# Performance work log

Measured on AMD Instinct MI355X. Metric: run time of the kernel, lower is better.

The kernel has to match this reference:

```python
import jax, jax.numpy as jnp
import numpy as np

IMG_W, IMG_H = 960.0, 512.0  # image_size from cfg


def setup_inputs() -> dict:
    B, N, J = 4, 5, 15
    Hh, Wh = 128, 240
    rng = np.random.default_rng(0)
    heatmaps = jnp.asarray(rng.random((N, B, J, Hh, Wh)).astype(np.float32))
    # rotations near identity (orthonormalized, det=+1)
    A = np.eye(3, dtype=np.float32) + 0.05 * rng.normal(size=(B, N, 3, 3)).astype(np.float32)
    Q = np.linalg.qr(A)[0]
    det = np.linalg.det(Q)
    Q[..., :, 0] = Q[..., :, 0] * det[..., None]
    R = jnp.asarray(Q.astype(np.float32))
    # cameras ~5m behind the volume so cam-z > 0 everywhere
    T = jnp.asarray((np.array([0.0, 0.0, -5000.0], np.float32) + 100.0 * rng.normal(size=(B, N, 3))).astype(np.float32))
    f = jnp.asarray((1000.0 + 20.0 * rng.normal(size=(B, N, 2))).astype(np.float32))
    c = jnp.asarray(np.tile(np.array([IMG_W / 2, IMG_H / 2], np.float32), (B, N, 1)))
    trans = jnp.asarray(np.tile(np.array([[1.0, 0.0, 0.0], [0.0, 1.0, 0.0]], np.float32), (B, N, 1, 1)))
    wh = jnp.asarray(np.tile(np.array([IMG_W, IMG_H], np.float32), (B, N, 1)))  # width,height = center*2
    gc = np.stack([rng.uniform(-500, 500, B), rng.uniform(-500, 500, B), np.full(B, 1000.0)], axis=1).astype(np.float32)
    grid_center = jnp.asarray(gc)
    return dict(heatmaps=heatmaps, R=R, T=T, f=f, c=c, trans=trans, wh=wh,
                grid_center=grid_center, gs_x=8000, gs_y=8000, gs_z=2000,
                cb_x=80, cb_y=80, cb_z=20)


def _bilinear(img, g):
    # img [J,H,W], g [P,2] in normalized coords; align_corners=True, zero padding
    Jn, H, W = img.shape
    x = (g[:, 0] + 1.0) * 0.5 * (W - 1)
    y = (g[:, 1] + 1.0) * 0.5 * (H - 1)
    x0 = jnp.floor(x)
    y0 = jnp.floor(y)
    wx = x - x0
    wy = y - y0

    def gather(xi, yi):
        valid = ((xi >= 0) & (xi <= W - 1) & (yi >= 0) & (yi <= H - 1)).astype(img.dtype)
        xc = jnp.clip(xi, 0, W - 1).astype(jnp.int32)
        yc = jnp.clip(yi, 0, H - 1).astype(jnp.int32)
        return img[:, yc, xc] * valid  # [J,P]

    return (gather(x0, y0) * (1 - wx) * (1 - wy) + gather(x0 + 1, y0) * wx * (1 - wy)
            + gather(x0, y0 + 1) * (1 - wx) * wy + gather(x0 + 1, y0 + 1) * wx * wy)


def _forward(heatmaps, R, T, f, c, trans, wh, grid_center, gs_x, gs_y, gs_z, cb_x, cb_y, cb_z):
    N, B, J, Hh, Wh = heatmaps.shape
    P = cb_x * cb_y * cb_z
    # compute_grid: world-space voxel centers per batch
    gx = jnp.linspace(-gs_x / 2, gs_x / 2, cb_x)
    gy = jnp.linspace(-gs_y / 2, gs_y / 2, cb_y)
    gz = jnp.linspace(-gs_z / 2, gs_z / 2, cb_z)
    mx, my, mz = jnp.meshgrid(gx, gy, gz, indexing='ij')
    base = jnp.stack([mx.ravel(), my.ravel(), mz.ravel()], axis=-1).astype(jnp.float32)  # [P,3]
    grids = base[None] + grid_center[:, None, :]                                         # [B,P,3]
    # world_to_pixel (pinhole): cam = R (X - T); pixel = f*cam_xy/cam_z + c
    diff = grids[:, None, :, :] - T[:, :, None, :]              # [B,N,P,3]
    cam = jnp.einsum('bnij,bnpj->bnpi', R, diff)                # [B,N,P,3]
    xy = cam[..., :2] / cam[..., 2:3] * f[:, :, None, :] + c[:, :, None, :]  # [B,N,P,2]
    width = wh[..., 0][:, :, None]
    height = wh[..., 1][:, :, None]
    bound = ((xy[..., 0] >= 0) & (xy[..., 1] >= 0) &
             (xy[..., 0] < width) & (xy[..., 1] < height)).astype(jnp.float32)  # [B,N,P]
    maxwh = jnp.maximum(width, height)[..., None]
    xy = jnp.clip(xy, -1.0, maxwh)
    # affine transform to model-input frame, then rescale to heatmap frame
    xy = jnp.einsum('bnij,bnpj->bnpi', trans[..., :2], xy) + trans[..., 2][:, :, None, :]
    xy = xy * jnp.array([Wh, Hh], jnp.float32) / jnp.array([IMG_W, IMG_H], jnp.float32)
    sg = jnp.clip(xy / jnp.array([Wh - 1, Hh - 1], jnp.float32) * 2.0 - 1.0, -1.1, 1.1)  # [B,N,P,2]
    imgs = jnp.transpose(heatmaps, (1, 0, 2, 3, 4)).reshape(B * N, J, Hh, Wh)
    samples = jax.vmap(_bilinear)(imgs, sg.reshape(B * N, P, 2))   # [B*N,J,P]
    cubes = jnp.transpose(samples.reshape(B, N, J, P), (0, 2, 3, 1))  # [B,J,P,N]
    wmask = jnp.transpose(bound, (0, 2, 1))[:, None]                  # [B,1,P,N]
    fused = jnp.sum(cubes * wmask, axis=-1) / (jnp.sum(wmask, axis=-1) + 1e-6)  # [B,J,P]
    fused = jnp.where(jnp.isnan(fused), 0.0, fused)
    fused = jnp.clip(fused, 0.0, 1.0).reshape(B, J, cb_x, cb_y, cb_z)
    return fused, grids


def reference(heatmaps, R, T, f, c, trans, wh, grid_center, gs_x, gs_y, gs_z, cb_x, cb_y, cb_z):
    return _forward(heatmaps, R, T, f, c, trans, wh, grid_center,
                    gs_x, gs_y, gs_z, cb_x, cb_y, cb_z)
```

## Files before the change

### kernel.cpp

```cpp
#include <hip/hip_runtime.h>
#include <hip/hip_fp16.h>

#define BB   4
#define NN   5
#define JJ   15
#define HHH  128
#define WHH  240
#define CBX  80
#define CBY  80
#define CBZ  20
#define PP   (CBX*CBY*CBZ)
#define HW   (HHH*WHH)
#define IMGW 960.0f
#define IMGH 512.0f
#define RECU 16


__global__ __launch_bounds__(256) void pack_kernel(
    const float* __restrict__ hm, unsigned int* __restrict__ ws)
{
    __shared__ float rows[JJ][WHH + 1];
    int bid = blockIdx.x;
    int n = bid % NN;
    int y = (bid / NN) % HHH;
    int b = bid / (NN * HHH);

    const float* src = hm + ((size_t)(n * BB + b) * JJ) * HW + y * WHH;
    for (int idx = threadIdx.x; idx < JJ * (WHH + 1); idx += 256) {
        int j = idx / (WHH + 1);
        int x = idx - j * (WHH + 1);
        int xs = min(x, WHH - 1);
        rows[j][x] = src[j * HW + xs];
    }
    __syncthreads();

    unsigned int* dst = ws + (size_t)((b * HHH + y) * NN + n) * WHH * RECU;
    for (int idx = threadIdx.x; idx < WHH * RECU; idx += 256) {
        int x = idx >> 4;
        int u = idx & 15;
        unsigned int val = 0u;
        if (u < JJ) {
            __half2 h = __halves2half2(__float2half_rn(rows[u][x]),
                                       __float2half_rn(rows[u][x + 1]));
            val = *reinterpret_cast<unsigned int*>(&h);
        }
        dst[idx] = val;
    }
}

__global__ __launch_bounds__(256) void project_kernel(
    const unsigned int* __restrict__ ws,
    const float* __restrict__ Rm,
    const float* __restrict__ Tv,
    const float* __restrict__ fv,
    const float* __restrict__ cv,
    const float* __restrict__ trans,
    const float* __restrict__ whv,
    const float* __restrict__ gcv,
    float* __restrict__ out)
{
    int t = blockIdx.x * blockDim.x + threadIdx.x;
    if (t >= BB * PP) return;
    int b = t / PP;
    int p = t - b * PP;
    int ix  = p / (CBY * CBZ);
    int rem = p - ix * (CBY * CBZ);
    int iy  = rem / CBZ;
    int iz  = rem - iy * CBZ;

    const float stx = 8000.0f / (CBX - 1);
    const float sty = 8000.0f / (CBY - 1);
    const float stz = 2000.0f / (CBZ - 1);
    float gx = -4000.0f + (float)ix * stx + gcv[b * 3 + 0];
    float gy = -4000.0f + (float)iy * sty + gcv[b * 3 + 1];
    float gz = -1000.0f + (float)iz * stz + gcv[b * 3 + 2];

    {
        float* grids_out = out + (size_t)BB * JJ * PP;
        size_t gb = (size_t)(b * PP + p) * 3;
        grids_out[gb + 0] = gx;
        grids_out[gb + 1] = gy;
        grids_out[gb + 2] = gz;
    }

    float cl0[NN], cr0[NN], cl1[NN], cr1[NN];
    int   r0[NN], r1[NN];
    float bnd[NN];
    float sumb = 0.0f;

    #pragma unroll
    for (int n = 0; n < NN; ++n) {
        int bn = b * NN + n;
        const float* R = Rm + bn * 9;
        float dx = gx - Tv[bn * 3 + 0];
        float dy = gy - Tv[bn * 3 + 1];
        float dz = gz - Tv[bn * 3 + 2];
        float cx = R[0] * dx + R[1] * dy + R[2] * dz;
        float cy = R[3] * dx + R[4] * dy + R[5] * dz;
        float cz = R[6] * dx + R[7] * dy + R[8] * dz;
        float inv = 1.0f / cz;
        float px = cx * inv * fv[bn * 2 + 0] + cv[bn * 2 + 0];
        float py = cy * inv * fv[bn * 2 + 1] + cv[bn * 2 + 1];
        float w = whv[bn * 2 + 0], h = whv[bn * 2 + 1];
        float bound = (px >= 0.0f && py >= 0.0f && px < w && py < h) ? 1.0f : 0.0f;
        float mwh = fmaxf(w, h);
        px = fminf(fmaxf(px, -1.0f), mwh);
        py = fminf(fmaxf(py, -1.0f), mwh);
        const float* tr = trans + bn * 6;
        float tx = tr[0] * px + tr[1] * py + tr[2];
        float ty = tr[3] * px + tr[4] * py + tr[5];
        tx *= (float)WHH / IMGW;
        ty *= (float)HHH / IMGH;
        float sgx = tx / (float)(WHH - 1) * 2.0f - 1.0f;
        float sgy = ty / (float)(HHH - 1) * 2.0f - 1.0f;
        sgx = fminf(fmaxf(sgx, -1.1f), 1.1f);
        sgy = fminf(fmaxf(sgy, -1.1f), 1.1f);
        float xx = (sgx + 1.0f) * 0.5f * (float)(WHH - 1);
        float yy = (sgy + 1.0f) * 0.5f * (float)(HHH - 1);
        float x0f = floorf(xx), y0f = floorf(yy);
        float wx = xx - x0f, wy = yy - y0f;
        int x0 = (int)x0f, y0 = (int)y0f;

        float axl, axr; int xb;
        if (x0 < 0) {
            axl = (x0 == -1) ? wx : 0.0f; axr = 0.0f; xb = 0;
        } else if (x0 >= WHH - 1) {
            axl = (x0 == WHH - 1) ? (1.0f - wx) : 0.0f; axr = 0.0f; xb = WHH - 1;
        } else {
            axl = 1.0f - wx; axr = wx; xb = x0;
        }

        float vy0 = (y0 >= 0 && y0 <= HHH - 1) ? 1.0f : 0.0f;
        float vy1 = (y0 + 1 >= 0 && y0 + 1 <= HHH - 1) ? 1.0f : 0.0f;
        int yc0 = min(max(y0, 0), HHH - 1);
        int yc1 = min(max(y0 + 1, 0), HHH - 1);
        float ay0 = (1.0f - wy) * vy0 * bound;
        float ay1 = wy * vy1 * bound;

        cl0[n] = axl * ay0;  cr0[n] = axr * ay0;
        cl1[n] = axl * ay1;  cr1[n] = axr * ay1;
        r0[n] = ((((b * HHH + yc0) * NN + n) * WHH) + xb) * RECU;
        r1[n] = ((((b * HHH + yc1) * NN + n) * WHH) + xb) * RECU;
        bnd[n] = bound;
        sumb += bound;
    }

    float acc[JJ];
    #pragma unroll
    for (int j = 0; j < JJ; ++j) acc[j] = 0.0f;

    #pragma unroll
    for (int n = 0; n < NN; ++n) {
        if (bnd[n] != 0.0f) {
            const uint4* q0 = reinterpret_cast<const uint4*>(ws + r0[n]);
            const uint4* q1 = reinterpret_cast<const uint4*>(ws + r1[n]);
            uint4 a0 = q0[0], a1 = q0[1], a2 = q0[2], a3 = q0[3];
            uint4 b0 = q1[0], b1 = q1[1], b2 = q1[2], b3 = q1[3];
            float c0l = cl0[n], c0r = cr0[n], c1l = cl1[n], c1r = cr1[n];
            unsigned int s0[16] = {a0.x,a0.y,a0.z,a0.w, a1.x,a1.y,a1.z,a1.w,
                                   a2.x,a2.y,a2.z,a2.w, a3.x,a3.y,a3.z,a3.w};
            unsigned int s1[16] = {b0.x,b0.y,b0.z,b0.w, b1.x,b1.y,b1.z,b1.w,
                                   b2.x,b2.y,b2.z,b2.w, b3.x,b3.y,b3.z,b3.w};
            #pragma unroll
            for (int j = 0; j < JJ; ++j) {
                __half2 h0 = *reinterpret_cast<__half2*>(&s0[j]);
                __half2 h1 = *reinterpret_cast<__half2*>(&s1[j]);
                float2 f0 = __half22float2(h0);
                float2 f1 = __half22float2(h1);
                acc[j] += c0l * f0.x + c0r * f0.y + c1l * f1.x + c1r * f1.y;
            }
        }
    }

    float denom = 1.0f / (sumb + 1e-6f);
    size_t outb = (size_t)b * JJ * PP + p;
    #pragma unroll
    for (int j = 0; j < JJ; ++j) {
        float v = acc[j] * denom;
        v = fminf(fmaxf(v, 0.0f), 1.0f);
        out[outb + (size_t)j * PP] = v;
    }
}

extern "C" void kernel_launch(void* const* d_in, const int* in_sizes, int n_in,
                              void* d_out, int out_size, void* d_ws, size_t ws_size,
                              hipStream_t stream) {
    const float* hm    = (const float*)d_in[0];
    const float* Rm    = (const float*)d_in[1];
    const float* Tv    = (const float*)d_in[2];
    const float* fv    = (const float*)d_in[3];
    const float* cv    = (const float*)d_in[4];
    const float* trans = (const float*)d_in[5];
    const float* whv   = (const float*)d_in[6];
    const float* gcv   = (const float*)d_in[7];
    float* out = (float*)d_out;
    unsigned int* ws = (unsigned int*)d_ws;

    pack_kernel<<<BB * HHH * NN, 256, 0, stream>>>(hm, ws);

    int total = BB * PP;
    int block = 256;
    int grid  = (total + block - 1) / block;
    project_kernel<<<grid, block, 0, stream>>>(ws, Rm, Tv, fv, cv, trans, whv, gcv, out);
}
```

Measured before the change: 153.5 us.

## Split joint channels across four threads per voxel in projection kernel

Each voxel is now handled by four threads, each responsible for four of the fifteen joint channels. Each thread loads one 16-byte vector per camera row instead of four. This cuts per-thread register pressure and raises the number of threads available to hide gather latency. In exchange, the projection math is repeated four times per voxel, and output stores become strided across lanes, since adjacent threads write different joint planes for the same voxel.

Measured after the change: 169.8 us. 10.7% more time.

```diff
diff --git a/kernel.cpp b/kernel.cpp
--- a/kernel.cpp
+++ b/kernel.cpp
@@ -59,10 +59,12 @@
     const float* __restrict__ gcv,
     float* __restrict__ out)
 {
-    int t = blockIdx.x * blockDim.x + threadIdx.x;
-    if (t >= BB * PP) return;
-    int b = t / PP;
-    int p = t - b * PP;
+    int tid = threadIdx.x;
+    int jg  = tid & 3;
+    int v   = tid >> 2;
+    int tvox = blockIdx.x * 64 + v;
+    int b = tvox / PP;
+    int p = tvox - b * PP;
     int ix  = p / (CBY * CBZ);
     int rem = p - ix * (CBY * CBZ);
     int iy  = rem / CBZ;
@@ -75,7 +77,7 @@
     float gy = -4000.0f + (float)iy * sty + gcv[b * 3 + 1];
     float gz = -1000.0f + (float)iz * stz + gcv[b * 3 + 2];
 
-    {
+    if (jg == 0) {
         float* grids_out = out + (size_t)BB * JJ * PP;
         size_t gb = (size_t)(b * PP + p) * 3;
         grids_out[gb + 0] = gx;
@@ -139,46 +141,53 @@
 
         cl0[n] = axl * ay0;  cr0[n] = axr * ay0;
         cl1[n] = axl * ay1;  cr1[n] = axr * ay1;
-        r0[n] = ((((b * HHH + yc0) * NN + n) * WHH) + xb) * RECU;
-        r1[n] = ((((b * HHH + yc1) * NN + n) * WHH) + xb) * RECU;
+        r0[n] = ((((b * HHH + yc0) * NN + n) * WHH) + xb) * RECU + jg * 4;
+        r1[n] = ((((b * HHH + yc1) * NN + n) * WHH) + xb) * RECU + jg * 4;
         bnd[n] = bound;
         sumb += bound;
     }
 
-    float acc[JJ];
-    #pragma unroll
-    for (int j = 0; j < JJ; ++j) acc[j] = 0.0f;
+    float acc0 = 0.0f, acc1 = 0.0f, acc2 = 0.0f, acc3 = 0.0f;
 
     #pragma unroll
     for (int n = 0; n < NN; ++n) {
         if (bnd[n] != 0.0f) {
-            const uint4* q0 = reinterpret_cast<const uint4*>(ws + r0[n]);
-            const uint4* q1 = reinterpret_cast<const uint4*>(ws + r1[n]);
-            uint4 a0 = q0[0], a1 = q0[1], a2 = q0[2], a3 = q0[3];
-            uint4 b0 = q1[0], b1 = q1[1], b2 = q1[2], b3 = q1[3];
+            uint4 a = *reinterpret_cast<const uint4*>(ws + r0[n]);
+            uint4 c = *reinterpret_cast<const uint4*>(ws + r1[n]);
             float c0l = cl0[n], c0r = cr0[n], c1l = cl1[n], c1r = cr1[n];
-            unsigned int s0[16] = {a0.x,a0.y,a0.z,a0.w, a1.x,a1.y,a1.z,a1.w,
-                                   a2.x,a2.y,a2.z,a2.w, a3.x,a3.y,a3.z,a3.w};
-            unsigned int s1[16] = {b0.x,b0.y,b0.z,b0.w, b1.x,b1.y,b1.z,b1.w,
-                                   b2.x,b2.y,b2.z,b2.w, b3.x,b3.y,b3.z,b3.w};
-            #pragma unroll
-            for (int j = 0; j < JJ; ++j) {
-                __half2 h0 = *reinterpret_cast<__half2*>(&s0[j]);
-                __half2 h1 = *reinterpret_cast<__half2*>(&s1[j]);
-                float2 f0 = __half22float2(h0);
-                float2 f1 = __half22float2(h1);
-                acc[j] += c0l * f0.x + c0r * f0.y + c1l * f1.x + c1r * f1.y;
-            }
+            float2 f;
+            f = __half22float2(*reinterpret_cast<__half2*>(&a.x));
+            acc0 += c0l * f.x + c0r * f.y;
+            f = __half22float2(*reinterpret_cast<__half2*>(&a.y));
+            acc1 += c0l * f.x + c0r * f.y;
+            f = __half22float2(*reinterpret_cast<__half2*>(&a.z));
+            acc2 += c0l * f.x + c0r * f.y;
+            f = __half22float2(*reinterpret_cast<__half2*>(&a.w));
+            acc3 += c0l * f.x + c0r * f.y;
+            f = __half22float2(*reinterpret_cast<__half2*>(&c.x));
+            acc0 += c1l * f.x + c1r * f.y;
+            f = __half22float2(*reinterpret_cast<__half2*>(&c.y));
+            acc1 += c1l * f.x + c1r * f.y;
+            f = __half22float2(*reinterpret_cast<__half2*>(&c.z));
+            acc2 += c1l * f.x + c1r * f.y;
+            f = __half22float2(*reinterpret_cast<__half2*>(&c.w));
+            acc3 += c1l * f.x + c1r * f.y;
         }
     }
 
     float denom = 1.0f / (sumb + 1e-6f);
     size_t outb = (size_t)b * JJ * PP + p;
-    #pragma unroll
-    for (int j = 0; j < JJ; ++j) {
-        float v = acc[j] * denom;
-        v = fminf(fmaxf(v, 0.0f), 1.0f);
-        out[outb + (size_t)j * PP] = v;
+    int j0 = jg * 4;
+    float vv;
+    vv = fminf(fmaxf(acc0 * denom, 0.0f), 1.0f);
+    out[outb + (size_t)(j0 + 0) * PP] = vv;
+    vv = fminf(fmaxf(acc1 * denom, 0.0f), 1.0f);
+    out[outb + (size_t)(j0 + 1) * PP] = vv;
+    vv = fminf(fmaxf(acc2 * denom, 0.0f), 1.0f);
+    out[outb + (size_t)(j0 + 2) * PP] = vv;
+    if (j0 + 3 < JJ) {
+        vv = fminf(fmaxf(acc3 * denom, 0.0f), 1.0f);
+        out[outb + (size_t)(j0 + 3) * PP] = vv;
     }
 }
 
@@ -198,8 +207,5 @@
 
     pack_kernel<<<BB * HHH * NN, 256, 0, stream>>>(hm, ws);
 
-    int total = BB * PP;
-    int block = 256;
-    int grid  = (total + block - 1) / block;
-    project_kernel<<<grid, block, 0, stream>>>(ws, Rm, Tv, fv, cv, trans, whv, gcv, out);
+    project_kernel<<<BB * PP / 64, 256, 0, stream>>>(ws, Rm, Tv, fv, cv, trans, whv, gcv, out);
 }
```
